# Performance work log

Hardware: AMD Instinct MI355X
Metric: run time of the kernel (lower is better)

Reference implementation:

```python
import jax, jax.numpy as jnp
import numpy as np
from functools import partial

N_NODES = 50000
N_EDGES = 600000
N_FEAT = 128
HID = [128, 64, 32, 16]
N_GRAPHS = 64
N_CLASSES = 10


def gcn_conv(x, W, b, src, dst, n_nodes):
    # PyG GCNConv: h = x @ W; propagate with symmetric norm over A + I; add bias.
    h = x @ W  # [N, out]
    ones = jnp.ones((src.shape[0],), dtype=x.dtype)
    deg = jax.ops.segment_sum(ones, dst, num_segments=n_nodes) + 1.0  # self-loop
    dinv = jax.lax.rsqrt(deg)
    coef = dinv[src] * dinv[dst]  # [E]
    agg = jax.ops.segment_sum(h[src] * coef[:, None], dst, num_segments=n_nodes)
    agg = agg + h * (dinv * dinv)[:, None]  # self-loop contribution
    return agg + b


def global_mean_pool(x, batch, n_graphs):
    s = jax.ops.segment_sum(x, batch, num_segments=n_graphs)
    cnt = jax.ops.segment_sum(jnp.ones((x.shape[0],), x.dtype), batch, num_segments=n_graphs)
    return s / jnp.maximum(cnt, 1.0)[:, None]


def setup_inputs() -> dict:
    key = jax.random.key(0)
    ks = jax.random.split(key, 16)
    x = jax.random.normal(ks[0], (N_NODES, N_FEAT), dtype=jnp.float32)
    edge_index = jax.random.randint(ks[1], (2, N_EDGES), 0, N_NODES, dtype=jnp.int64)
    batch = jnp.sort(jax.random.randint(ks[2], (N_NODES,), 0, N_GRAPHS, dtype=jnp.int64))

    def glorot(k, fan_in, fan_out):
        s = float(np.sqrt(6.0 / (fan_in + fan_out)))
        return jax.random.uniform(k, (fan_in, fan_out), jnp.float32, -s, s)

    dims = [N_FEAT] + HID
    params = {}
    for i in range(4):
        params[f"W{i+1}"] = glorot(ks[3 + i], dims[i], dims[i + 1])
        params[f"b{i+1}"] = jnp.zeros((dims[i + 1],), jnp.float32)
    params["Wlin"] = glorot(ks[7], HID[-1], N_CLASSES)
    params["blin"] = jnp.zeros((N_CLASSES,), jnp.float32)
    return {"x": x, "edge_index": edge_index, "batch": batch, **params}


def reference(x, edge_index, batch, W1, b1, W2, b2, W3, b3, W4, b4, Wlin, blin):
    src, dst = edge_index[0], edge_index[1]
    n = x.shape[0]
    h = jax.nn.relu(gcn_conv(x, W1, b1, src, dst, n))
    h = jax.nn.relu(gcn_conv(h, W2, b2, src, dst, n))
    h = jax.nn.relu(gcn_conv(h, W3, b3, src, dst, n))
    h = jax.nn.relu(gcn_conv(h, W4, b4, src, dst, n))
    g = global_mean_pool(h, batch, N_GRAPHS)  # [G, 16]
    return g @ Wlin + blin
```

## Files before the change

kernel.cpp:

```cpp
#include <hip/hip_runtime.h>
#include <hip/hip_bf16.h>


#define N_GRAPHS 64
#define N_CLASSES 10

typedef short bf8_t __attribute__((ext_vector_type(8)));
typedef float f4_t  __attribute__((ext_vector_type(4)));

__device__ __forceinline__ float b2f(unsigned int u) {
  return __uint_as_float(u << 16);
}
__device__ __forceinline__ unsigned short f2b(float f) {
  unsigned int x = __float_as_uint(f);
  x += 0x7fffu + ((x >> 16) & 1u);
  return (unsigned short)(x >> 16);
}

__device__ __forceinline__ void block_detect(const unsigned int* __restrict__ xraw,
    const unsigned int* __restrict__ eraw, int* f32, int* i64) {
  __shared__ int c_bf, c_nz;
  if (threadIdx.x == 0) { c_bf = 0; c_nz = 0; }
  __syncthreads();
  unsigned int d = xraw[threadIdx.x & 255];
  int e = (int)(((d & 0xffffu) >> 7) & 0xff);
  if (e >= 100 && e <= 140) atomicAdd(&c_bf, 1);
  if (eraw && threadIdx.x < 64 && eraw[2 * threadIdx.x + 1] != 0u) atomicAdd(&c_nz, 1);
  __syncthreads();
  *f32 = (c_bf < 150) ? 1 : 0;
  if (i64) *i64 = (c_nz == 0) ? 1 : 0;
}

struct WPtrs { const void* p[10]; };
static constexpr int WSEG[10] = {16384, 128, 8192, 64, 2048, 32, 512, 16, 160, 10};
static constexpr int WTOTAL   = 27546;
static constexpr int WOFF[10] = {0, 16384, 16512, 24704, 24768, 26816, 26848, 27360, 27376, 27536};

__global__ __launch_bounds__(256) void edge_atomic_kernel(
    const unsigned int* __restrict__ xraw, const int* __restrict__ eraw,
    int* __restrict__ deg, int* __restrict__ rank, int E) {
  int f32, i64;
  block_detect(xraw, (const unsigned int*)eraw, &f32, &i64);
  #pragma unroll
  for (int r = 0; r < 4; ++r) {
    int e = blockIdx.x * 1024 + r * 256 + threadIdx.x;
    if (e < E) {
      int d = i64 ? eraw[2 * (E + e)] : eraw[E + e];
      rank[e] = atomicAdd(&deg[d], 1);
    }
  }
}

__global__ __launch_bounds__(256) void scan_cvt_kernel(const int* __restrict__ deg,
    int* __restrict__ row_ptr, float* __restrict__ dinv,
    unsigned long long* __restrict__ desc, uint2* __restrict__ csr,
    const unsigned int* __restrict__ xraw, const int* __restrict__ eraw,
    WPtrs wp, unsigned short* __restrict__ wc,
    const int* __restrict__ braw, int* __restrict__ b32,
    unsigned short* __restrict__ xb,
    int nb, int XC, int BW, int n) {
  int f32, i64;
  block_detect(xraw, (const unsigned int*)eraw, &f32, &i64);
  const int bid = blockIdx.x;
  if (bid < nb) {
    __shared__ int ws[4];
    __shared__ int s_total;
    __shared__ unsigned int s_prev;
    const int b = bid, tid = threadIdx.x, lane = tid & 63, wv = tid >> 6;
    const int i = b * 256 + tid;
    int v = (i < n) ? (deg[i] + 1) : 0;
    int x = v;
    #pragma unroll
    for (int off = 1; off < 64; off <<= 1) {
      int y = __shfl_up(x, off, 64);
      if (lane >= off) x += y;
    }
    if (lane == 63) ws[wv] = x;
    __syncthreads();
    int wbase = 0;
    for (int w = 0; w < wv; ++w) wbase += ws[w];
    int incl = x + wbase;
    if (tid == 0) {
      int tot = ws[0] + ws[1] + ws[2] + ws[3];
      s_total = tot;
      unsigned long long st = (b == 0) ? (2ULL << 62) : (1ULL << 62);
      atomicExch(&desc[b], st | (unsigned long long)(unsigned int)tot);
      if (b == 0) s_prev = 0u;
    }
    __syncthreads();
    if (b > 0 && wv == 0) {
      unsigned int running = 0;
      int j = b - 1;
      while (true) {
        int idx = j - lane;
        unsigned long long d;
        if (idx >= 0) {
          do { d = atomicAdd(&desc[idx], 0ULL); } while ((d >> 62) == 0ULL);
        } else {
          d = (2ULL << 62);
        }
        unsigned long long ball = __ballot((d >> 62) == 2ULL);
        int fp = ball ? (__ffsll((unsigned long long)ball) - 1) : 64;
        unsigned int contrib = (lane <= fp) ? (unsigned int)(d & 0xffffffffULL) : 0u;
        #pragma unroll
        for (int o = 32; o; o >>= 1) contrib += __shfl_xor(contrib, o, 64);
        running += contrib;
        if (fp < 64) break;
        j -= 64;
      }
      if (lane == 0) {
        atomicExch(&desc[b], (2ULL << 62) |
                   (unsigned long long)(unsigned int)(running + (unsigned int)s_total));
        s_prev = running;
      }
    }
    __syncthreads();
    int tot = (int)s_prev + incl;
    if (i < n) {
      row_ptr[i + 1] = tot;
      float di = rsqrtf((float)v);
      dinv[i] = di;
      uint2 se;
      se.x = (unsigned int)i;
      se.y = __float_as_uint(di * di);
      csr[tot - v] = se;
    }
    if (i == 0) row_ptr[0] = 0;
  } else if (bid < nb + XC) {
    int i = (bid - nb) * 2048 + threadIdx.x * 8;
    if (i < n * 128) {
      if (f32) {
        float4 u0 = *(const float4*)((const float*)xraw + i);
        float4 u1 = *(const float4*)((const float*)xraw + i + 4);
        uint4 o;
        o.x = (unsigned int)f2b(u0.x) | ((unsigned int)f2b(u0.y) << 16);
        o.y = (unsigned int)f2b(u0.z) | ((unsigned int)f2b(u0.w) << 16);
        o.z = (unsigned int)f2b(u1.x) | ((unsigned int)f2b(u1.y) << 16);
        o.w = (unsigned int)f2b(u1.z) | ((unsigned int)f2b(u1.w) << 16);
        *(uint4*)&xb[i] = o;
      } else {
        *(uint4*)&xb[i] = *(const uint4*)((const unsigned short*)xraw + i);
      }
    }
  } else if (bid < nb + XC + BW) {
    int i = (bid - nb - XC) * 256 + threadIdx.x;
    if (i >= WTOTAL) return;
    int off = i, s = 0;
    #pragma unroll
    for (int t = 0; t < 10; ++t) {
      if (s == 0 && off >= WSEG[t]) { off -= WSEG[t]; } else if (s == 0) { s = t + 1; }
    }
    s -= 1;
    int soff = off;
    if ((s & 1) == 0 && s <= 6) {
      int KB, FOUT;
      if (s == 0)      { KB = 4; FOUT = 128; }
      else if (s == 2) { KB = 4; FOUT = 64; }
      else if (s == 4) { KB = 2; FOUT = 32; }
      else             { KB = 1; FOUT = 16; }
      int j = off & 7, l = (off >> 3) & 63, f = off >> 9;
      int ct = f / KB, kb = f - ct * KB;
      int k = kb * 32 + ((l >> 4) << 3) + j;
      int nn = ct * 16 + (l & 15);
      soff = k * FOUT + nn;
    }
    const void* p = wp.p[s];
    wc[WOFF[s] + off] = f32 ? f2b(((const float*)p)[soff])
                            : ((const unsigned short*)p)[soff];
  } else {
    int i = (bid - nb - XC - BW) * 256 + threadIdx.x;
    if (i < n) b32[i] = i64 ? braw[2 * i] : braw[i];
  }
}

__global__ __launch_bounds__(256) void fill_kernel(
    const int* __restrict__ eraw, const unsigned int* __restrict__ xraw,
    const int* __restrict__ row_ptr, const int* __restrict__ rank,
    const float* __restrict__ dinv, uint2* __restrict__ csr, int E) {
  int f32, i64;
  block_detect(xraw, (const unsigned int*)eraw, &f32, &i64);
  int e = blockIdx.x * 256 + threadIdx.x;
  if (e >= E) return;
  int s, d;
  if (i64) { s = eraw[2 * e]; d = eraw[2 * (E + e)]; }
  else     { s = eraw[e];     d = eraw[E + e]; }
  int pos = row_ptr[d] + 1 + rank[e];
  uint2 v;
  v.x = (unsigned int)s;
  v.y = __float_as_uint(dinv[s] * dinv[d]);
  csr[pos] = v;
}

template<int DW> struct UVec { unsigned int d[DW]; };
template<int DW>
__device__ __forceinline__ UVec<DW> uload(const unsigned int* p) {
  UVec<DW> r;
  if constexpr (DW == 4) { uint4 v = *(const uint4*)p; r.d[0]=v.x; r.d[1]=v.y; r.d[2]=v.z; r.d[3]=v.w; }
  else if constexpr (DW == 2) { uint2 v = *(const uint2*)p; r.d[0]=v.x; r.d[1]=v.y; }
  else { r.d[0] = *p; }
  return r;
}
template<int DW>
__device__ __forceinline__ void ustore(unsigned int* p, const UVec<DW>& v) {
  if constexpr (DW == 4) { *(uint4*)p = make_uint4(v.d[0], v.d[1], v.d[2], v.d[3]); }
  else if constexpr (DW == 2) { *(uint2*)p = make_uint2(v.d[0], v.d[1]); }
  else { *p = v.d[0]; }
}

template<int DW, int LPG>
__device__ __forceinline__ void gather_shfl(
    const unsigned int* __restrict__ H2, int FPD,
    const uint2* __restrict__ csr, int e0, int e1, int l, float* a) {
  for (int base = e0; base < e1; base += LPG) {
    int cnt = e1 - base < LPG ? e1 - base : LPG;
    uint2 my = csr[(base + l < e1) ? (base + l) : (e1 - 1)];
    for (int j0 = 0; j0 < cnt; j0 += 4) {
      int   sj[4];
      float cj[4];
      #pragma unroll
      for (int jj = 0; jj < 4; ++jj) {
        int j = j0 + jj;
        sj[jj] = __shfl((int)my.x, j & (LPG - 1), LPG);
        float cc = __uint_as_float(__shfl((int)my.y, j & (LPG - 1), LPG));
        cj[jj] = (j < cnt) ? cc : 0.f;
      }
      UVec<DW> v[4];
      #pragma unroll
      for (int jj = 0; jj < 4; ++jj)
        v[jj] = uload<DW>(H2 + (size_t)sj[jj] * FPD + l * DW);
      #pragma unroll
      for (int jj = 0; jj < 4; ++jj) {
        #pragma unroll
        for (int d = 0; d < DW; ++d) {
          a[2*d]   = fmaf(b2f(v[jj].d[d] & 0xffffu), cj[jj], a[2*d]);
          a[2*d+1] = fmaf(b2f(v[jj].d[d] >> 16),     cj[jj], a[2*d+1]);
        }
      }
    }
  }
}

__global__ __launch_bounds__(256) void aggemm0_kernel(
    const unsigned short* __restrict__ Xb,
    const int* __restrict__ row_ptr, const uint2* __restrict__ csr,
    const unsigned short* __restrict__ wc,
    unsigned short* __restrict__ Hout, int n) {
  constexpr int LPG = 16, DW = 4, LD = 136;
  __shared__ unsigned short T[16 * LD];
  __shared__ unsigned short T2[16 * LD];
  const int r = threadIdx.x / LPG, l = threadIdx.x % LPG;
  const int node0 = blockIdx.x * 16;
  const int g = node0 + r;
  UVec<DW> o;
  #pragma unroll
  for (int d = 0; d < DW; ++d) o.d[d] = 0u;
  if (g < n) {
    float a[2 * DW];
    #pragma unroll
    for (int d = 0; d < 2 * DW; ++d) a[d] = 0.f;
    gather_shfl<DW, LPG>((const unsigned int*)Xb, 64, csr,
                         row_ptr[g], row_ptr[g + 1], l, a);
    #pragma unroll
    for (int d = 0; d < DW; ++d)
      o.d[d] = (unsigned int)f2b(a[2*d]) | ((unsigned int)f2b(a[2*d+1]) << 16);
  }
  ustore<DW>((unsigned int*)&T[r * LD + l * DW * 2], o);
  __syncthreads();
  const int w = threadIdx.x >> 6;
  const int ll = threadIdx.x & 63;
  const int l15 = ll & 15, quad = ll >> 4;
  const unsigned short* W1f = wc + WOFF[0];
  const unsigned short* b1  = wc + WOFF[1];
  const unsigned short* W2f = wc + WOFF[2];
  #pragma unroll
  for (int c = 0; c < 2; ++c) {
    const int ct1 = w * 2 + c;
    f4_t acc = {0.f, 0.f, 0.f, 0.f};
    #pragma unroll
    for (int kb = 0; kb < 4; ++kb) {
      bf8_t afr = *(const bf8_t*)&T[l15 * LD + kb * 32 + quad * 8];
      bf8_t bfr = *(const bf8_t*)&W1f[((ct1 * 4 + kb) * 64 + ll) * 8];
      acc = __builtin_amdgcn_mfma_f32_16x16x32_bf16(afr, bfr, acc, 0, 0, 0);
    }
    float bv = b2f(b1[ct1 * 16 + l15]);
    #pragma unroll
    for (int rr = 0; rr < 4; ++rr)
      T2[(quad * 4 + rr) * LD + ct1 * 16 + l15] = f2b(fmaxf(acc[rr] + bv, 0.f));
  }
  __syncthreads();
  f4_t a2 = {0.f, 0.f, 0.f, 0.f};
  #pragma unroll
  for (int kb = 0; kb < 4; ++kb) {
    bf8_t afr = *(const bf8_t*)&T2[l15 * LD + kb * 32 + quad * 8];
    bf8_t bfr = *(const bf8_t*)&W2f[((w * 4 + kb) * 64 + ll) * 8];
    a2 = __builtin_amdgcn_mfma_f32_16x16x32_bf16(afr, bfr, a2, 0, 0, 0);
  }
  #pragma unroll
  for (int rr = 0; rr < 4; ++rr) {
    int node = node0 + quad * 4 + rr;
    if (node < n)
      Hout[(size_t)node * 64 + w * 16 + l15] = f2b(a2[rr]);
  }
}

template<int FIN, int FOUT, int LPG>
__global__ __launch_bounds__(256) void aggemm_kernel(
    const unsigned short* __restrict__ Hin,
    const int* __restrict__ row_ptr, const uint2* __restrict__ csr,
    const unsigned short* __restrict__ bias,
    const unsigned short* __restrict__ Wf, unsigned short* __restrict__ Hout, int n) {
  constexpr int DW  = FIN / LPG / 2;
  constexpr int NPB = 256 / LPG;
  constexpr int LD  = FIN + 8;
  constexpr int KB  = FIN / 32;
  constexpr int CT  = FOUT / 16;
  constexpr int MT  = NPB / 16;
  __shared__ unsigned short T[NPB * LD];
  const int r = threadIdx.x / LPG, l = threadIdx.x % LPG;
  const int node0 = blockIdx.x * NPB;
  const int g = node0 + r;
  UVec<DW> o;
  #pragma unroll
  for (int d = 0; d < DW; ++d) o.d[d] = 0u;
  if (g < n) {
    float a[2 * DW];
    #pragma unroll
    for (int d = 0; d < 2 * DW; ++d) a[d] = 0.f;
    gather_shfl<DW, LPG>((const unsigned int*)Hin, FIN / 2, csr,
                         row_ptr[g], row_ptr[g + 1], l, a);
    UVec<DW> bb = uload<DW>((const unsigned int*)bias + l * DW);
    #pragma unroll
    for (int d = 0; d < DW; ++d) {
      float lo = fmaxf(a[2*d]   + b2f(bb.d[d] & 0xffffu), 0.f);
      float hi = fmaxf(a[2*d+1] + b2f(bb.d[d] >> 16), 0.f);
      o.d[d] = (unsigned int)f2b(lo) | ((unsigned int)f2b(hi) << 16);
    }
  }
  ustore<DW>((unsigned int*)&T[r * LD + l * DW * 2], o);
  __syncthreads();
  const int w = threadIdx.x >> 6;
  if (w < MT * CT && node0 < n) {
    const int mt = w / CT, ct = w % CT;
    const int ll = threadIdx.x & 63;
    const int r16 = ll & 15, quad = ll >> 4;
    bf8_t afrag[KB], bfrag[KB];
    #pragma unroll
    for (int kb = 0; kb < KB; ++kb) {
      afrag[kb] = *(const bf8_t*)(&T[(mt * 16 + r16) * LD + quad * 8 + kb * 32]);
      bfrag[kb] = *(const bf8_t*)(Wf + ((ct * KB + kb) * 64 + ll) * 8);
    }
    f4_t acc = {0.f, 0.f, 0.f, 0.f};
    #pragma unroll
    for (int kb = 0; kb < KB; ++kb)
      acc = __builtin_amdgcn_mfma_f32_16x16x32_bf16(afrag[kb], bfrag[kb], acc, 0, 0, 0);
    #pragma unroll
    for (int rr = 0; rr < 4; ++rr) {
      int node = node0 + mt * 16 + quad * 4 + rr;
      if (node < n)
        Hout[(size_t)node * FOUT + ct * 16 + r16] = f2b(acc[rr]);
    }
  }
}

__global__ __launch_bounds__(256) void agg_pool_kernel(
    const unsigned short* __restrict__ Hin,
    const int* __restrict__ row_ptr, const uint2* __restrict__ csr,
    const unsigned short* __restrict__ bias,
    const int* __restrict__ batch, float* __restrict__ pooled,
    float* __restrict__ cnt, int n) {
  __shared__ float acc[N_GRAPHS * 16];
  __shared__ float ccnt[N_GRAPHS];
  for (int i = threadIdx.x; i < N_GRAPHS * 16; i += 256) acc[i] = 0.f;
  if (threadIdx.x < N_GRAPHS) ccnt[threadIdx.x] = 0.f;
  __syncthreads();
  const int r = threadIdx.x >> 3, l = threadIdx.x & 7;
  const int g = blockIdx.x * 32 + r;
  if (g < n) {
    const unsigned int* H2 = (const unsigned int*)Hin;
    float a0 = 0.f, a1 = 0.f;
    const int e0 = row_ptr[g], e1 = row_ptr[g + 1];
    for (int base = e0; base < e1; base += 8) {
      uint2 eb[8];
      #pragma unroll
      for (int j = 0; j < 8; ++j)
        eb[j] = csr[(base + j < e1) ? (base + j) : (e1 - 1)];
      float cj[8];
      unsigned int v[8];
      #pragma unroll
      for (int j = 0; j < 8; ++j)
        cj[j] = (base + j < e1) ? __uint_as_float(eb[j].y) : 0.f;
      #pragma unroll
      for (int j = 0; j < 8; ++j)
        v[j] = H2[(size_t)eb[j].x * 8 + l];
      #pragma unroll
      for (int j = 0; j < 8; ++j) {
        a0 = fmaf(b2f(v[j] & 0xffffu), cj[j], a0);
        a1 = fmaf(b2f(v[j] >> 16),     cj[j], a1);
      }
    }
    unsigned int bb = ((const unsigned int*)bias)[l];
    a0 = fmaxf(a0 + b2f(bb & 0xffffu), 0.f);
    a1 = fmaxf(a1 + b2f(bb >> 16), 0.f);
    int gb = batch[g];
    atomicAdd(&acc[gb * 16 + l * 2 + 0], a0);
    atomicAdd(&acc[gb * 16 + l * 2 + 1], a1);
    if (l == 0) atomicAdd(&ccnt[gb], 1.f);
  }
  __syncthreads();
  for (int i = threadIdx.x; i < N_GRAPHS * 16; i += 256)
    if (acc[i] != 0.f) atomicAdd(&pooled[i], acc[i]);
  if (threadIdx.x < N_GRAPHS && ccnt[threadIdx.x] != 0.f)
    atomicAdd(&cnt[threadIdx.x], ccnt[threadIdx.x]);
}

__global__ __launch_bounds__(256) void final_kernel(const float* __restrict__ pooled,
    const float* __restrict__ cnt, const unsigned short* __restrict__ wc,
    void* __restrict__ out, const unsigned int* __restrict__ xraw) {
  int f32;
  block_detect(xraw, nullptr, &f32, nullptr);
  int id = blockIdx.x * 256 + threadIdx.x;
  if (id >= N_GRAPHS * N_CLASSES) return;
  const unsigned short* Wlin = wc + WOFF[8];
  const unsigned short* blin = wc + WOFF[9];
  int g = id / N_CLASSES, c = id - g * N_CLASSES;
  float inv = 1.0f / fmaxf(cnt[g], 1.0f);
  float a = b2f(blin[c]);
  #pragma unroll
  for (int f = 0; f < 16; ++f)
    a = fmaf(pooled[g * 16 + f] * inv, b2f(Wlin[f * N_CLASSES + c]), a);
  if (f32) ((float*)out)[id] = a;
  else     ((unsigned short*)out)[id] = f2b(a);
}

extern "C" void kernel_launch(void* const* d_in, const int* in_sizes, int n_in,
                              void* d_out, int out_size, void* d_ws, size_t ws_size,
                              hipStream_t stream) {
  const unsigned int* xraw = (const unsigned int*)d_in[0];
  const int* eraw          = (const int*)d_in[1];
  const int* braw          = (const int*)d_in[2];

  const int N = in_sizes[2];
  const int E = in_sizes[1] / 2;
  const int nb = (N + 255) / 256;

  char* p = (char*)d_ws;
  auto alloc = [&](size_t bytes) -> void* {
    void* r = (void*)p;
    p += (bytes + 255) & ~(size_t)255;
    return r;
  };
  const size_t off_desc = ((size_t)N * 4 + 255) & ~(size_t)255;
  const size_t off_pool = (off_desc + (size_t)nb * 8 + 255) & ~(size_t)255;
  const size_t ztotal   = off_pool + (N_GRAPHS * 16 + N_GRAPHS) * 4;
  char* zbase = (char*)alloc(ztotal);
  int*   deg    = (int*)zbase;
  unsigned long long* desc = (unsigned long long*)(zbase + off_desc);
  float* pooled = (float*)(zbase + off_pool);
  float* cntf   = pooled + N_GRAPHS * 16;

  int*   row_ptr  = (int*)  alloc((size_t)(N + 1) * 4);
  int*   rank     = (int*)  alloc((size_t)E * 4);
  float* dinv     = (float*)alloc((size_t)N * 4);
  int*   batch32  = (int*)  alloc((size_t)N * 4);
  uint2* csr      = (uint2*)alloc((size_t)(E + N + 16) * 8);
  unsigned short* wcan  = (unsigned short*)alloc((size_t)WTOTAL * 2);
  unsigned short* xb    = (unsigned short*)alloc((size_t)N * 128 * 2);
  unsigned short* hbufA = (unsigned short*)alloc((size_t)N * 128 * 2);
  unsigned short* hbufB = (unsigned short*)alloc((size_t)N * 128 * 2);

  hipMemsetAsync(zbase, 0, ztotal, stream);

  WPtrs wp;
  for (int i = 0; i < 10; ++i) wp.p[i] = d_in[3 + i];

  const int BW  = (WTOTAL + 255) / 256;
  const int BB  = nb;
  const int BE  = (E + 255) / 256;
  const int BE4 = (E + 1023) / 1024;
  const int XC  = (N * 128 + 2047) / 2048;

  edge_atomic_kernel<<<BE4, 256, 0, stream>>>(xraw, eraw, deg, rank, E);

  scan_cvt_kernel<<<nb + XC + BW + BB, 256, 0, stream>>>(deg, row_ptr, dinv,
      desc, csr, xraw, eraw, wp, wcan, braw, batch32, xb, nb, XC, BW, N);

  const unsigned short* b2 = wcan + WOFF[3];
  const unsigned short* W3 = wcan + WOFF[4];
  const unsigned short* b3 = wcan + WOFF[5];
  const unsigned short* W4 = wcan + WOFF[6];
  const unsigned short* b4 = wcan + WOFF[7];

  fill_kernel<<<BE, 256, 0, stream>>>(eraw, xraw, row_ptr, rank, dinv, csr, E);

  aggemm0_kernel<<<(N + 15) / 16, 256, 0, stream>>>(
      xb, row_ptr, csr, wcan, hbufB, N);
  aggemm_kernel<64, 32, 8><<<(N + 31) / 32, 256, 0, stream>>>(
      hbufB, row_ptr, csr, b2, W3, hbufA, N);
  aggemm_kernel<32, 16, 8><<<(N + 31) / 32, 256, 0, stream>>>(
      hbufA, row_ptr, csr, b3, W4, hbufB, N);
  agg_pool_kernel<<<(N + 31) / 32, 256, 0, stream>>>(hbufB, row_ptr, csr, b4,
      batch32, pooled, cntf, N);

  final_kernel<<<(N_GRAPHS * N_CLASSES + 255) / 256, 256, 0, stream>>>(pooled, cntf, wcan, d_out, xraw);
}
```

Baseline: 212.8 us.

## Move x/weight conversion into the edge-degree kernel and split scan out

After: 207.8 us. 2.3% less time.

```diff
diff --git a/kernel.cpp b/kernel.cpp
--- a/kernel.cpp
+++ b/kernel.cpp
@@ -36,98 +36,26 @@
 static constexpr int WTOTAL   = 27546;
 static constexpr int WOFF[10] = {0, 16384, 16512, 24704, 24768, 26816, 26848, 27360, 27376, 27536};
 
-__global__ __launch_bounds__(256) void edge_atomic_kernel(
-    const unsigned int* __restrict__ xraw, const int* __restrict__ eraw,
-    int* __restrict__ deg, int* __restrict__ rank, int E) {
-  int f32, i64;
-  block_detect(xraw, (const unsigned int*)eraw, &f32, &i64);
-  #pragma unroll
-  for (int r = 0; r < 4; ++r) {
-    int e = blockIdx.x * 1024 + r * 256 + threadIdx.x;
-    if (e < E) {
-      int d = i64 ? eraw[2 * (E + e)] : eraw[E + e];
-      rank[e] = atomicAdd(&deg[d], 1);
-    }
-  }
-}
-
-__global__ __launch_bounds__(256) void scan_cvt_kernel(const int* __restrict__ deg,
-    int* __restrict__ row_ptr, float* __restrict__ dinv,
-    unsigned long long* __restrict__ desc, uint2* __restrict__ csr,
-    const unsigned int* __restrict__ xraw, const int* __restrict__ eraw,
-    WPtrs wp, unsigned short* __restrict__ wc,
+__global__ __launch_bounds__(256) void cvtwe_kernel(
+    const unsigned int* __restrict__ xraw, WPtrs wp, unsigned short* __restrict__ wc,
     const int* __restrict__ braw, int* __restrict__ b32,
+    const int* __restrict__ eraw, int* __restrict__ deg, int* __restrict__ rank,
     unsigned short* __restrict__ xb,
-    int nb, int XC, int BW, int n) {
+    int BE2, int XC, int BW, int n, int E) {
   int f32, i64;
   block_detect(xraw, (const unsigned int*)eraw, &f32, &i64);
   const int bid = blockIdx.x;
-  if (bid < nb) {
-    __shared__ int ws[4];
-    __shared__ int s_total;
-    __shared__ unsigned int s_prev;
-    const int b = bid, tid = threadIdx.x, lane = tid & 63, wv = tid >> 6;
-    const int i = b * 256 + tid;
-    int v = (i < n) ? (deg[i] + 1) : 0;
-    int x = v;
-    #pragma unroll
-    for (int off = 1; off < 64; off <<= 1) {
-      int y = __shfl_up(x, off, 64);
-      if (lane >= off) x += y;
-    }
-    if (lane == 63) ws[wv] = x;
-    __syncthreads();
-    int wbase = 0;
-    for (int w = 0; w < wv; ++w) wbase += ws[w];
-    int incl = x + wbase;
-    if (tid == 0) {
-      int tot = ws[0] + ws[1] + ws[2] + ws[3];
-      s_total = tot;
-      unsigned long long st = (b == 0) ? (2ULL << 62) : (1ULL << 62);
-      atomicExch(&desc[b], st | (unsigned long long)(unsigned int)tot);
-      if (b == 0) s_prev = 0u;
-    }
-    __syncthreads();
-    if (b > 0 && wv == 0) {
-      unsigned int running = 0;
-      int j = b - 1;
-      while (true) {
-        int idx = j - lane;
-        unsigned long long d;
-        if (idx >= 0) {
-          do { d = atomicAdd(&desc[idx], 0ULL); } while ((d >> 62) == 0ULL);
-        } else {
-          d = (2ULL << 62);
-        }
-        unsigned long long ball = __ballot((d >> 62) == 2ULL);
-        int fp = ball ? (__ffsll((unsigned long long)ball) - 1) : 64;
-        unsigned int contrib = (lane <= fp) ? (unsigned int)(d & 0xffffffffULL) : 0u;
-        #pragma unroll
-        for (int o = 32; o; o >>= 1) contrib += __shfl_xor(contrib, o, 64);
-        running += contrib;
-        if (fp < 64) break;
-        j -= 64;
+  if (bid < BE2) {
+    #pragma unroll
+    for (int r = 0; r < 2; ++r) {
+      int e = bid * 512 + r * 256 + threadIdx.x;
+      if (e < E) {
+        int d = i64 ? eraw[2 * (E + e)] : eraw[E + e];
+        rank[e] = atomicAdd(&deg[d], 1);
       }
-      if (lane == 0) {
-        atomicExch(&desc[b], (2ULL << 62) |
-                   (unsigned long long)(unsigned int)(running + (unsigned int)s_total));
-        s_prev = running;
-      }
-    }
-    __syncthreads();
-    int tot = (int)s_prev + incl;
-    if (i < n) {
-      row_ptr[i + 1] = tot;
-      float di = rsqrtf((float)v);
-      dinv[i] = di;
-      uint2 se;
-      se.x = (unsigned int)i;
-      se.y = __float_as_uint(di * di);
-      csr[tot - v] = se;
-    }
-    if (i == 0) row_ptr[0] = 0;
-  } else if (bid < nb + XC) {
-    int i = (bid - nb) * 2048 + threadIdx.x * 8;
+    }
+  } else if (bid < BE2 + XC) {
+    int i = (bid - BE2) * 2048 + threadIdx.x * 8;
     if (i < n * 128) {
       if (f32) {
         float4 u0 = *(const float4*)((const float*)xraw + i);
@@ -142,8 +70,8 @@
         *(uint4*)&xb[i] = *(const uint4*)((const unsigned short*)xraw + i);
       }
     }
-  } else if (bid < nb + XC + BW) {
-    int i = (bid - nb - XC) * 256 + threadIdx.x;
+  } else if (bid < BE2 + XC + BW) {
+    int i = (bid - BE2 - XC) * 256 + threadIdx.x;
     if (i >= WTOTAL) return;
     int off = i, s = 0;
     #pragma unroll
@@ -168,9 +96,77 @@
     wc[WOFF[s] + off] = f32 ? f2b(((const float*)p)[soff])
                             : ((const unsigned short*)p)[soff];
   } else {
-    int i = (bid - nb - XC - BW) * 256 + threadIdx.x;
+    int i = (bid - BE2 - XC - BW) * 256 + threadIdx.x;
     if (i < n) b32[i] = i64 ? braw[2 * i] : braw[i];
   }
+}
+
+__global__ __launch_bounds__(256) void scan_kernel(const int* __restrict__ deg,
+    int* __restrict__ row_ptr, float* __restrict__ dinv,
+    unsigned long long* __restrict__ desc, uint2* __restrict__ csr, int n) {
+  __shared__ int ws[4];
+  __shared__ int s_total;
+  __shared__ unsigned int s_prev;
+  const int b = blockIdx.x, tid = threadIdx.x, lane = tid & 63, wv = tid >> 6;
+  const int i = b * 256 + tid;
+  int v = (i < n) ? (deg[i] + 1) : 0;
+  int x = v;
+  #pragma unroll
+  for (int off = 1; off < 64; off <<= 1) {
+    int y = __shfl_up(x, off, 64);
+    if (lane >= off) x += y;
+  }
+  if (lane == 63) ws[wv] = x;
+  __syncthreads();
+  int wbase = 0;
+  for (int w = 0; w < wv; ++w) wbase += ws[w];
+  int incl = x + wbase;
+  if (tid == 0) {
+    int tot = ws[0] + ws[1] + ws[2] + ws[3];
+    s_total = tot;
+    unsigned long long st = (b == 0) ? (2ULL << 62) : (1ULL << 62);
+    atomicExch(&desc[b], st | (unsigned long long)(unsigned int)tot);
+    if (b == 0) s_prev = 0u;
+  }
+  __syncthreads();
+  if (b > 0 && wv == 0) {
+    unsigned int running = 0;
+    int j = b - 1;
+    while (true) {
+      int idx = j - lane;
+      unsigned long long d;
+      if (idx >= 0) {
+        do { d = atomicAdd(&desc[idx], 0ULL); } while ((d >> 62) == 0ULL);
+      } else {
+        d = (2ULL << 62);
+      }
+      unsigned long long ball = __ballot((d >> 62) == 2ULL);
+      int fp = ball ? (__ffsll((unsigned long long)ball) - 1) : 64;
+      unsigned int contrib = (lane <= fp) ? (unsigned int)(d & 0xffffffffULL) : 0u;
+      #pragma unroll
+      for (int o = 32; o; o >>= 1) contrib += __shfl_xor(contrib, o, 64);
+      running += contrib;
+      if (fp < 64) break;
+      j -= 64;
+    }
+    if (lane == 0) {
+      atomicExch(&desc[b], (2ULL << 62) |
+                 (unsigned long long)(unsigned int)(running + (unsigned int)s_total));
+      s_prev = running;
+    }
+  }
+  __syncthreads();
+  int tot = (int)s_prev + incl;
+  if (i < n) {
+    row_ptr[i + 1] = tot;
+    float di = rsqrtf((float)v);
+    dinv[i] = di;
+    uint2 se;
+    se.x = (unsigned int)i;
+    se.y = __float_as_uint(di * di);
+    csr[tot - v] = se;
+  }
+  if (i == 0) row_ptr[0] = 0;
 }
 
 __global__ __launch_bounds__(256) void fill_kernel(
@@ -476,13 +472,12 @@
   const int BW  = (WTOTAL + 255) / 256;
   const int BB  = nb;
   const int BE  = (E + 255) / 256;
-  const int BE4 = (E + 1023) / 1024;
+  const int BE2 = (E + 511) / 512;
   const int XC  = (N * 128 + 2047) / 2048;
-
-  edge_atomic_kernel<<<BE4, 256, 0, stream>>>(xraw, eraw, deg, rank, E);
-
-  scan_cvt_kernel<<<nb + XC + BW + BB, 256, 0, stream>>>(deg, row_ptr, dinv,
-      desc, csr, xraw, eraw, wp, wcan, braw, batch32, xb, nb, XC, BW, N);
+  cvtwe_kernel<<<BE2 + XC + BW + BB, 256, 0, stream>>>(xraw, wp, wcan,
+      braw, batch32, eraw, deg, rank, xb, BE2, XC, BW, N, E);
+
+  scan_kernel<<<nb, 256, 0, stream>>>(deg, row_ptr, dinv, desc, csr, N);
 
   const unsigned short* b2 = wcan + WOFF[3];
   const unsigned short* W3 = wcan + WOFF[4];
```
